# Kernel optimization log

Hardware: AMD Instinct MI355X
Metric: run time of the kernel (lower is better)

Reference implementation:

```python
import jax, jax.numpy as jnp
import numpy as np

B, S, IN_DIM = 2, 2048, 1024
DIMS, QH, KVH = 1024, 16, 4
HD = DIMS // QH          # head_dims = 64
G = QH // KVH            # groups = 4


def setup_inputs() -> dict:
    key = jax.random.key(0)
    k1, k2, k3, k4, k5, k6 = jax.random.split(key, 6)
    scale = 0.02
    q_in = jax.random.normal(k1, (B, S, IN_DIM), dtype=jnp.float32)
    kv_in = jax.random.normal(k2, (B, S, IN_DIM), dtype=jnp.float32)
    # causal mask (True = attend)
    mask = jnp.tril(jnp.ones((S, S), dtype=bool))
    Wq = jax.random.normal(k3, (IN_DIM, QH, HD), dtype=jnp.float32) * scale
    Wk = jax.random.normal(k4, (IN_DIM, KVH, HD), dtype=jnp.float32) * scale
    Wv = jax.random.normal(k5, (IN_DIM, KVH, HD), dtype=jnp.float32) * scale
    Wo = jax.random.normal(k6, (KVH * HD, IN_DIM), dtype=jnp.float32) * scale
    return {"q_in": q_in, "kv_in": kv_in, "mask": mask,
            "Wq": Wq, "Wk": Wk, "Wv": Wv, "Wo": Wo}


def reference(q_in, kv_in, mask, Wq, Wk, Wv, Wo):
    b, s, _ = q_in.shape
    # projections (DenseGeneral, no bias)
    q = jnp.einsum('bsi,ihd->bshd', q_in, Wq)   # [B,S,QH,HD]
    k = jnp.einsum('bsi,ihd->bshd', kv_in, Wk)  # [B,S,KVH,HD]
    v = jnp.einsum('bsi,ihd->bshd', kv_in, Wv)  # [B,S,KVH,HD]
    # rearrange '... s (h g) d -> ... g h s d' with g=G (h outer, g inner),
    # then einsum '... g h s d, ... h a d -> ... h s a' sums over g.
    # Equivalent (and cheaper): sum q over the group axis first.
    q_g = q.reshape(b, s, KVH, G, HD).sum(axis=3)        # [B,S,KVH,HD]
    q_g = jnp.transpose(q_g, (0, 2, 1, 3))               # [B,KVH,S,HD]
    k = jnp.transpose(k, (0, 2, 1, 3))                   # [B,KVH,S,HD]
    v = jnp.transpose(v, (0, 2, 1, 3))                   # [B,KVH,S,HD]
    scores = jnp.einsum('bhsd,bhad->bhsa', q_g, k)       # [B,KVH,S,S]
    scores = jnp.where(mask[None, None, :, :], scores, -jnp.inf)
    attn = jax.nn.softmax(scores / (HD ** 0.5), axis=-1)
    out = jnp.einsum('bhsa,bhad->bhsd', attn, v)         # [B,KVH,S,HD]
    out = jnp.transpose(out, (0, 2, 1, 3)).reshape(b, s, KVH * HD)
    return out @ Wo                                      # [B,S,IN_DIM]
```

## Files before the change

kernel.cpp:

```cpp
#include <hip/hip_runtime.h>
#include <hip/hip_bf16.h>

#define SS 2048
#define NSPLIT 8

typedef __attribute__((ext_vector_type(8))) short bf16x8;
typedef __attribute__((ext_vector_type(4))) float f32x4;

__device__ __forceinline__ short f2bf(float f){
    unsigned u = __float_as_uint(f);
    u += 0x7fff + ((u >> 16) & 1);
    return (short)(u >> 16);
}
__device__ __forceinline__ float bf2f(short s){
    return __uint_as_float(((unsigned)(unsigned short)s) << 16);
}
__device__ __forceinline__ void gload_lds16(const void* g, void* l){
    __builtin_amdgcn_global_load_lds((const __attribute__((address_space(1))) void*)g,
                                     (__attribute__((address_space(3))) void*)l, 16, 0, 0);
}

__global__ __launch_bounds__(256) void k_prep_w(const float* __restrict__ Wq,
                                                const float* __restrict__ Wk,
                                                const float* __restrict__ Wv,
                                                const float* __restrict__ Wo,
                                                const float* __restrict__ q_in,
                                                const float* __restrict__ kv_in,
                                                short* __restrict__ WcatT,
                                                short* __restrict__ WoT,
                                                short* __restrict__ Xb){
    const int bx = blockIdx.x;
    if (bx >= 256) {
        const int b2 = bx - 256;
        const float* src = (b2 < 128) ? q_in : kv_in;
        short* dst = Xb + ((b2 < 128) ? (size_t)0 : (size_t)4194304);
        const int tg = (b2 & 127) * 256 + threadIdx.x;
        #pragma unroll
        for (int j = 0; j < 8; ++j) {
            size_t off = (size_t)tg * 16 + (size_t)j * 524288;
            float4 f0 = *(const float4*)(src + off);
            float4 f1 = *(const float4*)(src + off + 4);
            float4 f2 = *(const float4*)(src + off + 8);
            float4 f3 = *(const float4*)(src + off + 12);
            short t[16];
            t[0]=f2bf(f0.x); t[1]=f2bf(f0.y); t[2]=f2bf(f0.z); t[3]=f2bf(f0.w);
            t[4]=f2bf(f1.x); t[5]=f2bf(f1.y); t[6]=f2bf(f1.z); t[7]=f2bf(f1.w);
            t[8]=f2bf(f2.x); t[9]=f2bf(f2.y); t[10]=f2bf(f2.z); t[11]=f2bf(f2.w);
            t[12]=f2bf(f3.x); t[13]=f2bf(f3.y); t[14]=f2bf(f3.z); t[15]=f2bf(f3.w);
            *(bf16x8*)(dst + off)     = *(bf16x8*)&t[0];
            *(bf16x8*)(dst + off + 8) = *(bf16x8*)&t[8];
        }
        return;
    }
    __shared__ float Ts[64][65];
    const int r  = threadIdx.x >> 2;
    const int cq = (threadIdx.x & 3) * 16;
    if (bx < 192) {
        const int ktile = bx & 15, ntile = bx >> 4;
        const int k0 = ktile * 64, n0 = ntile * 64;
        if (ntile < 4) {
            const float* base = Wq + (size_t)(k0 + r) * 1024 + ntile * 256;
            #pragma unroll
            for (int i = 0; i < 16; i += 4) {
                float4 a = *(const float4*)(base + cq + i);
                float4 b = *(const float4*)(base + 64 + cq + i);
                float4 c = *(const float4*)(base + 128 + cq + i);
                float4 d = *(const float4*)(base + 192 + cq + i);
                Ts[r][cq+i]   = 0.125f * (a.x + b.x + c.x + d.x);
                Ts[r][cq+i+1] = 0.125f * (a.y + b.y + c.y + d.y);
                Ts[r][cq+i+2] = 0.125f * (a.z + b.z + c.z + d.z);
                Ts[r][cq+i+3] = 0.125f * (a.w + b.w + c.w + d.w);
            }
        } else {
            const float* W = (ntile < 8) ? Wk : Wv;
            const float* base = W + (size_t)(k0 + r) * 256 + (ntile & 3) * 64;
            #pragma unroll
            for (int i = 0; i < 16; i += 4) {
                float4 a = *(const float4*)(base + cq + i);
                Ts[r][cq+i] = a.x; Ts[r][cq+i+1] = a.y;
                Ts[r][cq+i+2] = a.z; Ts[r][cq+i+3] = a.w;
            }
        }
        __syncthreads();
        short tmp[16];
        #pragma unroll
        for (int i = 0; i < 16; ++i) tmp[i] = f2bf(Ts[cq+i][r]);
        short* dst = WcatT + (size_t)(n0 + r) * 1024 + k0 + cq;
        *(bf16x8*)dst       = *(bf16x8*)&tmp[0];
        *(bf16x8*)(dst + 8) = *(bf16x8*)&tmp[8];
    } else {
        const int b2 = bx - 192;
        const int ktile = b2 & 3, ntile = b2 >> 2;
        const int k0 = ktile * 64, n0 = ntile * 64;
        const float* base = Wo + (size_t)(k0 + r) * 1024 + n0;
        #pragma unroll
        for (int i = 0; i < 16; i += 4) {
            float4 a = *(const float4*)(base + cq + i);
            Ts[r][cq+i] = a.x; Ts[r][cq+i+1] = a.y;
            Ts[r][cq+i+2] = a.z; Ts[r][cq+i+3] = a.w;
        }
        __syncthreads();
        short tmp[16];
        #pragma unroll
        for (int i = 0; i < 16; ++i) tmp[i] = f2bf(Ts[cq+i][r]);
        short* dst = WoT + (size_t)(n0 + r) * 256 + k0 + cq;
        *(bf16x8*)dst       = *(bf16x8*)&tmp[0];
        *(bf16x8*)(dst + 8) = *(bf16x8*)&tmp[8];
    }
}

__global__ __launch_bounds__(256) void k_gemm1(const short* __restrict__ Xb,
                                               const short* __restrict__ WcatT,
                                               short* __restrict__ pqk,
                                               short* __restrict__ vt){
    const int m0 = blockIdx.x * 128;
    const int n0 = blockIdx.y * 128;
    const short* X = Xb + ((n0 < 256) ? (size_t)0 : (size_t)4194304);
    const int tid = threadIdx.x;
    const int wave = tid >> 6, lane = tid & 63, quad = lane >> 4, l16 = lane & 15;
    const int wrow = (wave & 1) * 64, wcol = (wave >> 1) * 64;

    __shared__ char SMEM[65536];

    f32x4 acc[4][4];
    #pragma unroll
    for (int tm = 0; tm < 4; ++tm)
        #pragma unroll
        for (int tn = 0; tn < 4; ++tn) acc[tm][tn] = f32x4{0.f,0.f,0.f,0.f};

    const int lr8 = lane >> 3;
    const int sb  = ((lane & 7) * 16) ^ (lr8 << 4);
    const char* Abase = (const char*)X     + (size_t)m0 * 2048;
    const char* Bbase = (const char*)WcatT + (size_t)n0 * 2048;

    auto STAGE = [&](int buf, int k0) {
        #pragma unroll
        for (int j = 0; j < 4; ++j) {
            const int row = wave * 32 + j * 8 + lr8;
            const size_t goff = (size_t)row * 2048 + (size_t)k0 * 2 + sb;
            gload_lds16(Abase + goff, SMEM + buf * 32768 + wave * 4096 + j * 1024);
            gload_lds16(Bbase + goff, SMEM + buf * 32768 + 16384 + wave * 4096 + j * 1024);
        }
    };

    STAGE(0, 0);
    for (int k0 = 0; k0 < 1024; k0 += 64) {
        __syncthreads();
        const int cur = (k0 >> 6) & 1;
        if (k0 + 64 < 1024) STAGE(cur ^ 1, k0 + 64);
        #pragma unroll
        for (int ks = 0; ks < 2; ++ks) {
            const int cswz = ((ks * 64 + quad * 16) ^ ((l16 & 7) << 4));
            bf16x8 a[4];
            #pragma unroll
            for (int tm = 0; tm < 4; ++tm) {
                const int R = wrow + tm * 16 + l16;
                a[tm] = *(const bf16x8*)(SMEM + cur * 32768 + R * 128 + cswz);
            }
            #pragma unroll
            for (int tn = 0; tn < 4; ++tn) {
                const int R2 = wcol + tn * 16 + l16;
                bf16x8 b = *(const bf16x8*)(SMEM + cur * 32768 + 16384 + R2 * 128 + cswz);
                #pragma unroll
                for (int tm = 0; tm < 4; ++tm)
                    acc[tm][tn] = __builtin_amdgcn_mfma_f32_16x16x32_bf16(a[tm], b, acc[tm][tn], 0, 0, 0);
            }
        }
    }
    __syncthreads();

    if (n0 < 512) {
        #pragma unroll
        for (int tm = 0; tm < 4; ++tm) {
            const int mrow = m0 + wrow + tm * 16 + quad * 4;
            #pragma unroll
            for (int tn = 0; tn < 4; ++tn) {
                const int col = n0 + wcol + tn * 16 + l16;
                #pragma unroll
                for (int rg = 0; rg < 4; ++rg)
                    pqk[(size_t)(mrow + rg) * 512 + col] = f2bf(acc[tm][tn][rg]);
            }
        }
    } else {
        short* SM16 = (short*)SMEM;
        #pragma unroll
        for (int tm = 0; tm < 4; ++tm) {
            const int ml = wrow + tm * 16 + quad * 4;
            #pragma unroll
            for (int tn = 0; tn < 4; ++tn) {
                const int cl = wcol + tn * 16 + l16;
                #pragma unroll
                for (int rg = 0; rg < 4; ++rg)
                    SM16[cl * 136 + ml + rg] = f2bf(acc[tm][tn][rg]);
            }
        }
        __syncthreads();
        const int row  = tid >> 1;
        const int half = tid & 1;
        const int colv = (n0 - 512) + row;
        const int vh = colv >> 6, d = colv & 63;
        const int batch = m0 >> 11;
        const int s0 = (m0 & 2047) + half * 64;
        short* dst = vt + ((size_t)((batch * 4 + vh) * 64 + d)) * 2048 + s0;
        const short* src = &SM16[row * 136 + half * 64];
        #pragma unroll
        for (int i = 0; i < 64; i += 8)
            *(bf16x8*)(dst + i) = *(const bf16x8*)(src + i);
    }
}

__global__ __launch_bounds__(256) void k_attn4(const short* __restrict__ pqk,
                                               const short* __restrict__ vt,
                                               short* __restrict__ Op,
                                               float* __restrict__ Lp){
    const int bx = blockIdx.x;
    const int qt = 31 - (bx / NSPLIT);
    const int s  = bx - (bx / NSPLIT) * NSPLIT;
    const int kv = blockIdx.y, batch = blockIdx.z;
    const int tid = threadIdx.x;
    const int wave = tid >> 6, lane = tid & 63, quad = lane >> 4, l16 = lane & 15;
    const int r = tid >> 2, c = (tid & 3) * 16;
    const int part = (((batch * 4 + kv) * 32 + qt) * NSPLIT + s);

    __shared__ short Ks[64][72];
    __shared__ short Vs[64][72];
    __shared__ short Ps[64][72];

    const size_t qrow = (size_t)(batch * SS + qt * 64 + wave * 16 + l16);
    bf16x8 aq0 = *(const bf16x8*)(pqk + qrow * 512 + kv * 64 + quad * 8);
    bf16x8 aq1 = *(const bf16x8*)(pqk + qrow * 512 + kv * 64 + 32 + quad * 8);

    f32x4 accO[4];
    #pragma unroll
    for (int t = 0; t < 4; ++t) accO[t] = f32x4{0.f, 0.f, 0.f, 0.f};
    float lrow[4] = {0.f, 0.f, 0.f, 0.f};

    bf16x8 rk0, rk1, rv0, rv1;
    int kt = s;
    if (kt <= qt) {
        const short* ksrc = pqk + (size_t)(batch * SS + kt * 64 + r) * 512 + 256 + kv * 64 + c;
        rk0 = *(const bf16x8*)ksrc; rk1 = *(const bf16x8*)(ksrc + 8);
        const short* vsrc = vt + ((size_t)((batch * 4 + kv) * 64 + r)) * 2048 + kt * 64 + c;
        rv0 = *(const bf16x8*)vsrc; rv1 = *(const bf16x8*)(vsrc + 8);
    }
    for (; kt <= qt; kt += NSPLIT) {
        *(bf16x8*)&Ks[r][c]     = rk0;
        *(bf16x8*)&Ks[r][c + 8] = rk1;
        *(bf16x8*)&Vs[r][c]     = rv0;
        *(bf16x8*)&Vs[r][c + 8] = rv1;
        __syncthreads();
        if (kt + NSPLIT <= qt) {
            const short* ksrc = pqk + (size_t)(batch * SS + (kt + NSPLIT) * 64 + r) * 512 + 256 + kv * 64 + c;
            rk0 = *(const bf16x8*)ksrc; rk1 = *(const bf16x8*)(ksrc + 8);
            const short* vsrc = vt + ((size_t)((batch * 4 + kv) * 64 + r)) * 2048 + (kt + NSPLIT) * 64 + c;
            rv0 = *(const bf16x8*)vsrc; rv1 = *(const bf16x8*)(vsrc + 8);
        }

        f32x4 sc[4];
        #pragma unroll
        for (int t = 0; t < 4; ++t) sc[t] = f32x4{0.f, 0.f, 0.f, 0.f};
        #pragma unroll
        for (int ks = 0; ks < 2; ++ks) {
            bf16x8 a = ks ? aq1 : aq0;
            #pragma unroll
            for (int t = 0; t < 4; ++t) {
                bf16x8 b = *(bf16x8*)&Ks[t * 16 + l16][ks * 32 + quad * 8];
                sc[t] = __builtin_amdgcn_mfma_f32_16x16x32_bf16(a, b, sc[t], 0, 0, 0);
            }
        }
        if (kt == qt) {
            #pragma unroll
            for (int t = 0; t < 4; ++t) {
                int colg = t * 16 + l16;
                #pragma unroll
                for (int rg = 0; rg < 4; ++rg)
                    if (colg > wave * 16 + quad * 4 + rg) sc[t][rg] = -1e30f;
            }
        }
        #pragma unroll
        for (int t = 0; t < 4; ++t) {
            #pragma unroll
            for (int rg = 0; rg < 4; ++rg) {
                float p = __expf(sc[t][rg]);
                lrow[rg] += p;
                Ps[wave * 16 + quad * 4 + rg][t * 16 + l16] = f2bf(p);
            }
        }
        #pragma unroll
        for (int ks = 0; ks < 2; ++ks) {
            bf16x8 ap = *(bf16x8*)&Ps[wave * 16 + l16][ks * 32 + quad * 8];
            #pragma unroll
            for (int t = 0; t < 4; ++t) {
                bf16x8 bv = *(bf16x8*)&Vs[t * 16 + l16][ks * 32 + quad * 8];
                accO[t] = __builtin_amdgcn_mfma_f32_16x16x32_bf16(ap, bv, accO[t], 0, 0, 0);
            }
        }
        __syncthreads();
    }
    #pragma unroll
    for (int rg = 0; rg < 4; ++rg) {
        float l = lrow[rg];
        l += __shfl_xor(l, 1);
        l += __shfl_xor(l, 2);
        l += __shfl_xor(l, 4);
        l += __shfl_xor(l, 8);
        lrow[rg] = l;
    }
    #pragma unroll
    for (int rg = 0; rg < 4; ++rg) {
        int row = wave * 16 + quad * 4 + rg;
        #pragma unroll
        for (int t = 0; t < 4; ++t)
            Op[(size_t)part * 4096 + row * 64 + t * 16 + l16] = f2bf(accO[t][rg]);
    }
    if (l16 == 0) {
        #pragma unroll
        for (int rg = 0; rg < 4; ++rg)
            Lp[part * 64 + (wave * 16 + quad * 4 + rg)] = lrow[rg];
    }
}

__global__ __launch_bounds__(256) void k_combine(const short* __restrict__ Op,
                                                 const float* __restrict__ Lp,
                                                 short* __restrict__ ao){
    const int qt = blockIdx.x, kv = blockIdx.y, batch = blockIdx.z;
    const int tid = threadIdx.x;
    const int rr = tid >> 2, cs = (tid & 3) * 16;
    const int pbase = ((batch * 4 + kv) * 32 + qt) * NSPLIT;
    float lsum = 0.f;
    #pragma unroll
    for (int i = 0; i < NSPLIT; ++i) lsum += Lp[(pbase + i) * 64 + rr];
    float inv = 1.f / lsum;
    float o[16];
    #pragma unroll
    for (int j = 0; j < 16; ++j) o[j] = 0.f;
    #pragma unroll
    for (int i = 0; i < NSPLIT; ++i) {
        const short* src = Op + (size_t)(pbase + i) * 4096 + rr * 64 + cs;
        bf16x8 v0 = *(const bf16x8*)src;
        bf16x8 v1 = *(const bf16x8*)(src + 8);
        #pragma unroll
        for (int j = 0; j < 8; ++j) { o[j] += bf2f(v0[j]); o[j + 8] += bf2f(v1[j]); }
    }
    short* dst = ao + (size_t)(batch * SS + qt * 64 + rr) * 256 + kv * 64 + cs;
    #pragma unroll
    for (int j = 0; j < 16; ++j)
        dst[j] = f2bf(o[j] * inv);
}

__global__ __launch_bounds__(256) void k_gemm2(const short* __restrict__ ao,
                                               const short* __restrict__ WoT,
                                               float* __restrict__ out){
    const int m0 = blockIdx.x * 128;
    const int n0 = blockIdx.y * 128;
    const int tid = threadIdx.x;
    const int wave = tid >> 6, lane = tid & 63, quad = lane >> 4, l16 = lane & 15;
    const int wrow = (wave & 1) * 64, wcol = (wave >> 1) * 64;
    const int r = tid >> 2, cc = (tid & 3) * 16;

    __shared__ short As[128][72];
    __shared__ short Bs[128][72];

    f32x4 acc[4][4];
    #pragma unroll
    for (int tm = 0; tm < 4; ++tm)
        #pragma unroll
        for (int tn = 0; tn < 4; ++tn) acc[tm][tn] = f32x4{0.f,0.f,0.f,0.f};

    bf16x8 ra0, ra1, ra2, ra3, rb0, rb1, rb2, rb3;
    {
        const short* a0 = ao + (size_t)(m0 + r) * 256 + cc;
        const short* a1 = a0 + (size_t)64 * 256;
        const short* b0 = WoT + (size_t)(n0 + r) * 256 + cc;
        const short* b1 = b0 + (size_t)64 * 256;
        ra0 = *(const bf16x8*)a0; ra1 = *(const bf16x8*)(a0 + 8);
        ra2 = *(const bf16x8*)a1; ra3 = *(const bf16x8*)(a1 + 8);
        rb0 = *(const bf16x8*)b0; rb1 = *(const bf16x8*)(b0 + 8);
        rb2 = *(const bf16x8*)b1; rb3 = *(const bf16x8*)(b1 + 8);
    }
    for (int k0 = 0; k0 < 256; k0 += 64) {
        *(bf16x8*)&As[r][cc]          = ra0;
        *(bf16x8*)&As[r][cc + 8]      = ra1;
        *(bf16x8*)&As[r + 64][cc]     = ra2;
        *(bf16x8*)&As[r + 64][cc + 8] = ra3;
        *(bf16x8*)&Bs[r][cc]          = rb0;
        *(bf16x8*)&Bs[r][cc + 8]      = rb1;
        *(bf16x8*)&Bs[r + 64][cc]     = rb2;
        *(bf16x8*)&Bs[r + 64][cc + 8] = rb3;
        __syncthreads();
        if (k0 + 64 < 256) {
            const short* a0 = ao + (size_t)(m0 + r) * 256 + k0 + 64 + cc;
            const short* a1 = a0 + (size_t)64 * 256;
            const short* b0 = WoT + (size_t)(n0 + r) * 256 + k0 + 64 + cc;
            const short* b1 = b0 + (size_t)64 * 256;
            ra0 = *(const bf16x8*)a0; ra1 = *(const bf16x8*)(a0 + 8);
            ra2 = *(const bf16x8*)a1; ra3 = *(const bf16x8*)(a1 + 8);
            rb0 = *(const bf16x8*)b0; rb1 = *(const bf16x8*)(b0 + 8);
            rb2 = *(const bf16x8*)b1; rb3 = *(const bf16x8*)(b1 + 8);
        }
        #pragma unroll
        for (int ks = 0; ks < 2; ++ks) {
            bf16x8 a[4];
            #pragma unroll
            for (int tm = 0; tm < 4; ++tm)
                a[tm] = *(bf16x8*)&As[wrow + tm * 16 + l16][ks * 32 + quad * 8];
            #pragma unroll
            for (int tn = 0; tn < 4; ++tn) {
                bf16x8 b = *(bf16x8*)&Bs[wcol + tn * 16 + l16][ks * 32 + quad * 8];
                #pragma unroll
                for (int tm = 0; tm < 4; ++tm)
                    acc[tm][tn] = __builtin_amdgcn_mfma_f32_16x16x32_bf16(a[tm], b, acc[tm][tn], 0, 0, 0);
            }
        }
        __syncthreads();
    }
    #pragma unroll
    for (int tm = 0; tm < 4; ++tm) {
        const int mrow = m0 + wrow + tm * 16 + quad * 4;
        #pragma unroll
        for (int tn = 0; tn < 4; ++tn) {
            const int col = n0 + wcol + tn * 16 + l16;
            #pragma unroll
            for (int rg = 0; rg < 4; ++rg)
                out[(size_t)(mrow + rg) * 1024 + col] = acc[tm][tn][rg];
        }
    }
}

extern "C" void kernel_launch(void* const* d_in, const int* in_sizes, int n_in,
                              void* d_out, int out_size, void* d_ws, size_t ws_size,
                              hipStream_t stream) {
    const float* q_in  = (const float*)d_in[0];
    const float* kv_in = (const float*)d_in[1];
    int wqi = 3;
    for (int i = 2; i < n_in; ++i)
        if (in_sizes[i] == 1024 * 16 * 64) { wqi = i; break; }
    const float* Wq = (const float*)d_in[wqi];
    const float* Wk = (const float*)d_in[wqi + 1];
    const float* Wv = (const float*)d_in[wqi + 2];
    const float* Wo = (const float*)d_in[wqi + 3];
    float* out = (float*)d_out;

    char* ws = (char*)d_ws;
    short* WcatT = (short*)(ws);
    short* WoT   = (short*)(ws + 1572864);
    short* ao    = (short*)(ws + 2097152);
    short* pqk   = (short*)(ws + 4194304);
    short* vt    = (short*)(ws + 8388608);
    float* Lp    = (float*)(ws + 10485760);
    short* Op    = (short*)(ws + 33554432);
    short* Xb    = (short*)(ws + 50331648);

    hipLaunchKernelGGL(k_prep_w,  dim3(512),     dim3(256), 0, stream,
                       Wq, Wk, Wv, Wo, q_in, kv_in, WcatT, WoT, Xb);
    hipLaunchKernelGGL(k_gemm1,   dim3(32, 6),   dim3(256), 0, stream,
                       Xb, WcatT, pqk, vt);
    hipLaunchKernelGGL(k_attn4,   dim3(32 * NSPLIT, 4, 2), dim3(256), 0, stream,
                       pqk, vt, Op, Lp);
    hipLaunchKernelGGL(k_combine, dim3(32, 4, 2), dim3(256), 0, stream,
                       Op, Lp, ao);
    hipLaunchKernelGGL(k_gemm2,   dim3(32, 8),   dim3(256), 0, stream,
                       ao, WoT, out);
}
```

Before: 146.6 us.

## Remove split-KV attention and combine kernel, normalize output inside attention

Drops the split-K/V scheme: each block now handles one query tile, loops over all causal key tiles and writes normalized output straight into the attention buffer. This removes the separate combine kernel along with the write and re-read of the partial output and row-sum buffers. In exchange the grid shrinks from 2048 to 256 blocks, and under the causal mask the last query tiles run up to 32 serial iterations, so load balance and latency hiding may get worse.

```diff
diff --git a/kernel.cpp b/kernel.cpp
--- a/kernel.cpp
+++ b/kernel.cpp
@@ -2,7 +2,6 @@
 #include <hip/hip_bf16.h>
 
 #define SS 2048
-#define NSPLIT 8
 
 typedef __attribute__((ext_vector_type(8))) short bf16x8;
 typedef __attribute__((ext_vector_type(4))) float f32x4;
@@ -209,18 +208,14 @@
     }
 }
 
-__global__ __launch_bounds__(256) void k_attn4(const short* __restrict__ pqk,
-                                               const short* __restrict__ vt,
-                                               short* __restrict__ Op,
-                                               float* __restrict__ Lp){
-    const int bx = blockIdx.x;
-    const int qt = 31 - (bx / NSPLIT);
-    const int s  = bx - (bx / NSPLIT) * NSPLIT;
+__global__ __launch_bounds__(256) void k_attn(const short* __restrict__ pqk,
+                                              const short* __restrict__ vt,
+                                              short* __restrict__ ao){
+    const int qt = blockIdx.x;
     const int kv = blockIdx.y, batch = blockIdx.z;
     const int tid = threadIdx.x;
     const int wave = tid >> 6, lane = tid & 63, quad = lane >> 4, l16 = lane & 15;
     const int r = tid >> 2, c = (tid & 3) * 16;
-    const int part = (((batch * 4 + kv) * 32 + qt) * NSPLIT + s);
 
     __shared__ short Ks[64][72];
     __shared__ short Vs[64][72];
@@ -236,23 +231,22 @@
     float lrow[4] = {0.f, 0.f, 0.f, 0.f};
 
     bf16x8 rk0, rk1, rv0, rv1;
-    int kt = s;
-    if (kt <= qt) {
-        const short* ksrc = pqk + (size_t)(batch * SS + kt * 64 + r) * 512 + 256 + kv * 64 + c;
+    {
+        const short* ksrc = pqk + (size_t)(batch * SS + r) * 512 + 256 + kv * 64 + c;
         rk0 = *(const bf16x8*)ksrc; rk1 = *(const bf16x8*)(ksrc + 8);
-        const short* vsrc = vt + ((size_t)((batch * 4 + kv) * 64 + r)) * 2048 + kt * 64 + c;
+        const short* vsrc = vt + ((size_t)((batch * 4 + kv) * 64 + r)) * 2048 + c;
         rv0 = *(const bf16x8*)vsrc; rv1 = *(const bf16x8*)(vsrc + 8);
     }
-    for (; kt <= qt; kt += NSPLIT) {
+    for (int kt = 0; kt <= qt; ++kt) {
         *(bf16x8*)&Ks[r][c]     = rk0;
         *(bf16x8*)&Ks[r][c + 8] = rk1;
         *(bf16x8*)&Vs[r][c]     = rv0;
         *(bf16x8*)&Vs[r][c + 8] = rv1;
         __syncthreads();
-        if (kt + NSPLIT <= qt) {
-            const short* ksrc = pqk + (size_t)(batch * SS + (kt + NSPLIT) * 64 + r) * 512 + 256 + kv * 64 + c;
+        if (kt + 1 <= qt) {
+            const short* ksrc = pqk + (size_t)(batch * SS + (kt + 1) * 64 + r) * 512 + 256 + kv * 64 + c;
             rk0 = *(const bf16x8*)ksrc; rk1 = *(const bf16x8*)(ksrc + 8);
-            const short* vsrc = vt + ((size_t)((batch * 4 + kv) * 64 + r)) * 2048 + (kt + NSPLIT) * 64 + c;
+            const short* vsrc = vt + ((size_t)((batch * 4 + kv) * 64 + r)) * 2048 + (kt + 1) * 64 + c;
             rv0 = *(const bf16x8*)vsrc; rv1 = *(const bf16x8*)(vsrc + 8);
         }
 
@@ -304,48 +298,16 @@
         l += __shfl_xor(l, 2);
         l += __shfl_xor(l, 4);
         l += __shfl_xor(l, 8);
-        lrow[rg] = l;
+        lrow[rg] = 1.f / l;
     }
     #pragma unroll
     for (int rg = 0; rg < 4; ++rg) {
-        int row = wave * 16 + quad * 4 + rg;
+        const int row = qt * 64 + wave * 16 + quad * 4 + rg;
+        short* dst = ao + (size_t)(batch * SS + row) * 256 + kv * 64;
         #pragma unroll
         for (int t = 0; t < 4; ++t)
-            Op[(size_t)part * 4096 + row * 64 + t * 16 + l16] = f2bf(accO[t][rg]);
-    }
-    if (l16 == 0) {
-        #pragma unroll
-        for (int rg = 0; rg < 4; ++rg)
-            Lp[part * 64 + (wave * 16 + quad * 4 + rg)] = lrow[rg];
-    }
-}
-
-__global__ __launch_bounds__(256) void k_combine(const short* __restrict__ Op,
-                                                 const float* __restrict__ Lp,
-                                                 short* __restrict__ ao){
-    const int qt = blockIdx.x, kv = blockIdx.y, batch = blockIdx.z;
-    const int tid = threadIdx.x;
-    const int rr = tid >> 2, cs = (tid & 3) * 16;
-    const int pbase = ((batch * 4 + kv) * 32 + qt) * NSPLIT;
-    float lsum = 0.f;
-    #pragma unroll
-    for (int i = 0; i < NSPLIT; ++i) lsum += Lp[(pbase + i) * 64 + rr];
-    float inv = 1.f / lsum;
-    float o[16];
-    #pragma unroll
-    for (int j = 0; j < 16; ++j) o[j] = 0.f;
-    #pragma unroll
-    for (int i = 0; i < NSPLIT; ++i) {
-        const short* src = Op + (size_t)(pbase + i) * 4096 + rr * 64 + cs;
-        bf16x8 v0 = *(const bf16x8*)src;
-        bf16x8 v1 = *(const bf16x8*)(src + 8);
-        #pragma unroll
-        for (int j = 0; j < 8; ++j) { o[j] += bf2f(v0[j]); o[j + 8] += bf2f(v1[j]); }
-    }
-    short* dst = ao + (size_t)(batch * SS + qt * 64 + rr) * 256 + kv * 64 + cs;
-    #pragma unroll
-    for (int j = 0; j < 16; ++j)
-        dst[j] = f2bf(o[j] * inv);
+            dst[t * 16 + l16] = f2bf(accO[t][rg] * lrow[rg]);
+    }
 }
 
 __global__ __launch_bounds__(256) void k_gemm2(const short* __restrict__ ao,
@@ -447,18 +409,14 @@
     short* ao    = (short*)(ws + 2097152);
     short* pqk   = (short*)(ws + 4194304);
     short* vt    = (short*)(ws + 8388608);
-    float* Lp    = (float*)(ws + 10485760);
-    short* Op    = (short*)(ws + 33554432);
     short* Xb    = (short*)(ws + 50331648);
 
     hipLaunchKernelGGL(k_prep_w,  dim3(512),     dim3(256), 0, stream,
                        Wq, Wk, Wv, Wo, q_in, kv_in, WcatT, WoT, Xb);
     hipLaunchKernelGGL(k_gemm1,   dim3(32, 6),   dim3(256), 0, stream,
                        Xb, WcatT, pqk, vt);
-    hipLaunchKernelGGL(k_attn4,   dim3(32 * NSPLIT, 4, 2), dim3(256), 0, stream,
-                       pqk, vt, Op, Lp);
-    hipLaunchKernelGGL(k_combine, dim3(32, 4, 2), dim3(256), 0, stream,
-                       Op, Lp, ao);
+    hipLaunchKernelGGL(k_attn,    dim3(32, 4, 2), dim3(256), 0, stream,
+                       pqk, vt, ao);
     hipLaunchKernelGGL(k_gemm2,   dim3(32, 8),   dim3(256), 0, stream,
                        ao, WoT, out);
 }
```

After: 154.0 us. 5.0% more time.

## Fuse split-KV combine into attention via last-block atomic counter

Applied to the files above, without the earlier changes.

Removes the separate combine kernel launch: each attention block increments a per-query-tile atomic counter after writing its partial output, and the last finishing split reduces all partials and writes the normalized result. Counters are zeroed in the prep kernel. This saves a kernel launch and its dependency gap, at the cost of a threadfence plus atomic per block and a serial tail in the last block of each group.

```diff
diff --git a/kernel.cpp b/kernel.cpp
--- a/kernel.cpp
+++ b/kernel.cpp
@@ -28,9 +28,11 @@
                                                 const float* __restrict__ kv_in,
                                                 short* __restrict__ WcatT,
                                                 short* __restrict__ WoT,
-                                                short* __restrict__ Xb){
+                                                short* __restrict__ Xb,
+                                                unsigned* __restrict__ cnt){
     const int bx = blockIdx.x;
     if (bx >= 256) {
+        if (bx == 256 && threadIdx.x < 256) cnt[threadIdx.x] = 0u;
         const int b2 = bx - 256;
         const float* src = (b2 < 128) ? q_in : kv_in;
         short* dst = Xb + ((b2 < 128) ? (size_t)0 : (size_t)4194304);
@@ -212,7 +214,9 @@
 __global__ __launch_bounds__(256) void k_attn4(const short* __restrict__ pqk,
                                                const short* __restrict__ vt,
                                                short* __restrict__ Op,
-                                               float* __restrict__ Lp){
+                                               float* __restrict__ Lp,
+                                               unsigned* __restrict__ cnt,
+                                               short* __restrict__ ao){
     const int bx = blockIdx.x;
     const int qt = 31 - (bx / NSPLIT);
     const int s  = bx - (bx / NSPLIT) * NSPLIT;
@@ -220,11 +224,13 @@
     const int tid = threadIdx.x;
     const int wave = tid >> 6, lane = tid & 63, quad = lane >> 4, l16 = lane & 15;
     const int r = tid >> 2, c = (tid & 3) * 16;
-    const int part = (((batch * 4 + kv) * 32 + qt) * NSPLIT + s);
+    const int grp  = ((batch * 4 + kv) * 32 + qt);
+    const int part = grp * NSPLIT + s;
 
     __shared__ short Ks[64][72];
     __shared__ short Vs[64][72];
     __shared__ short Ps[64][72];
+    __shared__ int s_old;
 
     const size_t qrow = (size_t)(batch * SS + qt * 64 + wave * 16 + l16);
     bf16x8 aq0 = *(const bf16x8*)(pqk + qrow * 512 + kv * 64 + quad * 8);
@@ -318,34 +324,35 @@
         for (int rg = 0; rg < 4; ++rg)
             Lp[part * 64 + (wave * 16 + quad * 4 + rg)] = lrow[rg];
     }
-}
-
-__global__ __launch_bounds__(256) void k_combine(const short* __restrict__ Op,
-                                                 const float* __restrict__ Lp,
-                                                 short* __restrict__ ao){
-    const int qt = blockIdx.x, kv = blockIdx.y, batch = blockIdx.z;
-    const int tid = threadIdx.x;
-    const int rr = tid >> 2, cs = (tid & 3) * 16;
-    const int pbase = ((batch * 4 + kv) * 32 + qt) * NSPLIT;
-    float lsum = 0.f;
-    #pragma unroll
-    for (int i = 0; i < NSPLIT; ++i) lsum += Lp[(pbase + i) * 64 + rr];
-    float inv = 1.f / lsum;
-    float o[16];
-    #pragma unroll
-    for (int j = 0; j < 16; ++j) o[j] = 0.f;
-    #pragma unroll
-    for (int i = 0; i < NSPLIT; ++i) {
-        const short* src = Op + (size_t)(pbase + i) * 4096 + rr * 64 + cs;
-        bf16x8 v0 = *(const bf16x8*)src;
-        bf16x8 v1 = *(const bf16x8*)(src + 8);
-        #pragma unroll
-        for (int j = 0; j < 8; ++j) { o[j] += bf2f(v0[j]); o[j + 8] += bf2f(v1[j]); }
-    }
-    short* dst = ao + (size_t)(batch * SS + qt * 64 + rr) * 256 + kv * 64 + cs;
-    #pragma unroll
-    for (int j = 0; j < 16; ++j)
-        dst[j] = f2bf(o[j] * inv);
+
+    __threadfence();
+    __syncthreads();
+    if (tid == 0) s_old = (int)atomicAdd(&cnt[grp], 1u);
+    __syncthreads();
+    if (s_old == NSPLIT - 1) {
+        __threadfence();
+        const int rr = tid >> 2, cs = (tid & 3) * 16;
+        const int pbase = grp * NSPLIT;
+        float lsum = 0.f;
+        #pragma unroll
+        for (int i = 0; i < NSPLIT; ++i) lsum += Lp[(pbase + i) * 64 + rr];
+        float inv = 1.f / lsum;
+        float o[16];
+        #pragma unroll
+        for (int j = 0; j < 16; ++j) o[j] = 0.f;
+        #pragma unroll
+        for (int i = 0; i < NSPLIT; ++i) {
+            const short* src = Op + (size_t)(pbase + i) * 4096 + rr * 64 + cs;
+            bf16x8 v0 = *(const bf16x8*)src;
+            bf16x8 v1 = *(const bf16x8*)(src + 8);
+            #pragma unroll
+            for (int j = 0; j < 8; ++j) { o[j] += bf2f(v0[j]); o[j + 8] += bf2f(v1[j]); }
+        }
+        short* dst = ao + (size_t)(batch * SS + qt * 64 + rr) * 256 + kv * 64 + cs;
+        #pragma unroll
+        for (int j = 0; j < 16; ++j)
+            dst[j] = f2bf(o[j] * inv);
+    }
 }
 
 __global__ __launch_bounds__(256) void k_gemm2(const short* __restrict__ ao,
@@ -442,23 +449,22 @@
     float* out = (float*)d_out;
 
     char* ws = (char*)d_ws;
-    short* WcatT = (short*)(ws);
-    short* WoT   = (short*)(ws + 1572864);
-    short* ao    = (short*)(ws + 2097152);
-    short* pqk   = (short*)(ws + 4194304);
-    short* vt    = (short*)(ws + 8388608);
-    float* Lp    = (float*)(ws + 10485760);
-    short* Op    = (short*)(ws + 33554432);
-    short* Xb    = (short*)(ws + 50331648);
+    short* WcatT    = (short*)(ws);
+    short* WoT      = (short*)(ws + 1572864);
+    short* ao       = (short*)(ws + 2097152);
+    short* pqk      = (short*)(ws + 4194304);
+    short* vt       = (short*)(ws + 8388608);
+    float* Lp       = (float*)(ws + 10485760);
+    unsigned* cnt   = (unsigned*)(ws + 11534336);
+    short* Op       = (short*)(ws + 33554432);
+    short* Xb       = (short*)(ws + 50331648);
 
     hipLaunchKernelGGL(k_prep_w,  dim3(512),     dim3(256), 0, stream,
-                       Wq, Wk, Wv, Wo, q_in, kv_in, WcatT, WoT, Xb);
+                       Wq, Wk, Wv, Wo, q_in, kv_in, WcatT, WoT, Xb, cnt);
     hipLaunchKernelGGL(k_gemm1,   dim3(32, 6),   dim3(256), 0, stream,
                        Xb, WcatT, pqk, vt);
     hipLaunchKernelGGL(k_attn4,   dim3(32 * NSPLIT, 4, 2), dim3(256), 0, stream,
-                       pqk, vt, Op, Lp);
-    hipLaunchKernelGGL(k_combine, dim3(32, 4, 2), dim3(256), 0, stream,
-                       Op, Lp, ao);
+                       pqk, vt, Op, Lp, cnt, ao);
     hipLaunchKernelGGL(k_gemm2,   dim3(32, 8),   dim3(256), 0, stream,
                        ao, WoT, out);
 }
```

After: 479.3 us. 227% more time.

## Load K/V MFMA fragments directly from global memory, dropping LDS staging and barriers

Applied to the files above, without the earlier changes.

The attention kernel no longer stages K and V tiles in shared memory. Each wave now reads its K and V MFMA operand fragments straight from global memory, which removes both per-iteration __syncthreads. The P tile stays in LDS but is only touched by its own wave. In exchange, every wave fetches the same K/V data separately (roughly four times the cache traffic), the reads are strided rather than coalesced, and the register prefetch of the next tile is gone, so load latency sits inside the loop.

```diff
diff --git a/kernel.cpp b/kernel.cpp
--- a/kernel.cpp
+++ b/kernel.cpp
@@ -219,43 +219,24 @@
     const int kv = blockIdx.y, batch = blockIdx.z;
     const int tid = threadIdx.x;
     const int wave = tid >> 6, lane = tid & 63, quad = lane >> 4, l16 = lane & 15;
-    const int r = tid >> 2, c = (tid & 3) * 16;
     const int part = (((batch * 4 + kv) * 32 + qt) * NSPLIT + s);
 
-    __shared__ short Ks[64][72];
-    __shared__ short Vs[64][72];
     __shared__ short Ps[64][72];
 
     const size_t qrow = (size_t)(batch * SS + qt * 64 + wave * 16 + l16);
     bf16x8 aq0 = *(const bf16x8*)(pqk + qrow * 512 + kv * 64 + quad * 8);
     bf16x8 aq1 = *(const bf16x8*)(pqk + qrow * 512 + kv * 64 + 32 + quad * 8);
 
+    const short* Kb = pqk + (size_t)(batch * SS) * 512 + 256 + kv * 64
+                    + (size_t)(l16) * 512 + quad * 8;
+    const short* Vb = vt + ((size_t)((batch * 4 + kv) * 64 + l16)) * 2048 + quad * 8;
+
     f32x4 accO[4];
     #pragma unroll
     for (int t = 0; t < 4; ++t) accO[t] = f32x4{0.f, 0.f, 0.f, 0.f};
     float lrow[4] = {0.f, 0.f, 0.f, 0.f};
 
-    bf16x8 rk0, rk1, rv0, rv1;
-    int kt = s;
-    if (kt <= qt) {
-        const short* ksrc = pqk + (size_t)(batch * SS + kt * 64 + r) * 512 + 256 + kv * 64 + c;
-        rk0 = *(const bf16x8*)ksrc; rk1 = *(const bf16x8*)(ksrc + 8);
-        const short* vsrc = vt + ((size_t)((batch * 4 + kv) * 64 + r)) * 2048 + kt * 64 + c;
-        rv0 = *(const bf16x8*)vsrc; rv1 = *(const bf16x8*)(vsrc + 8);
-    }
-    for (; kt <= qt; kt += NSPLIT) {
-        *(bf16x8*)&Ks[r][c]     = rk0;
-        *(bf16x8*)&Ks[r][c + 8] = rk1;
-        *(bf16x8*)&Vs[r][c]     = rv0;
-        *(bf16x8*)&Vs[r][c + 8] = rv1;
-        __syncthreads();
-        if (kt + NSPLIT <= qt) {
-            const short* ksrc = pqk + (size_t)(batch * SS + (kt + NSPLIT) * 64 + r) * 512 + 256 + kv * 64 + c;
-            rk0 = *(const bf16x8*)ksrc; rk1 = *(const bf16x8*)(ksrc + 8);
-            const short* vsrc = vt + ((size_t)((batch * 4 + kv) * 64 + r)) * 2048 + (kt + NSPLIT) * 64 + c;
-            rv0 = *(const bf16x8*)vsrc; rv1 = *(const bf16x8*)(vsrc + 8);
-        }
-
+    for (int kt = s; kt <= qt; kt += NSPLIT) {
         f32x4 sc[4];
         #pragma unroll
         for (int t = 0; t < 4; ++t) sc[t] = f32x4{0.f, 0.f, 0.f, 0.f};
@@ -264,10 +245,16 @@
             bf16x8 a = ks ? aq1 : aq0;
             #pragma unroll
             for (int t = 0; t < 4; ++t) {
-                bf16x8 b = *(bf16x8*)&Ks[t * 16 + l16][ks * 32 + quad * 8];
+                bf16x8 b = *(const bf16x8*)(Kb + (size_t)(kt * 64 + t * 16) * 512 + ks * 32);
                 sc[t] = __builtin_amdgcn_mfma_f32_16x16x32_bf16(a, b, sc[t], 0, 0, 0);
             }
         }
+        bf16x8 bv[2][4];
+        #pragma unroll
+        for (int ks = 0; ks < 2; ++ks)
+            #pragma unroll
+            for (int t = 0; t < 4; ++t)
+                bv[ks][t] = *(const bf16x8*)(Vb + (size_t)(t * 16) * 2048 + kt * 64 + ks * 32);
         if (kt == qt) {
             #pragma unroll
             for (int t = 0; t < 4; ++t) {
@@ -290,12 +277,9 @@
         for (int ks = 0; ks < 2; ++ks) {
             bf16x8 ap = *(bf16x8*)&Ps[wave * 16 + l16][ks * 32 + quad * 8];
             #pragma unroll
-            for (int t = 0; t < 4; ++t) {
-                bf16x8 bv = *(bf16x8*)&Vs[t * 16 + l16][ks * 32 + quad * 8];
-                accO[t] = __builtin_amdgcn_mfma_f32_16x16x32_bf16(ap, bv, accO[t], 0, 0, 0);
-            }
-        }
-        __syncthreads();
+            for (int t = 0; t < 4; ++t)
+                accO[t] = __builtin_amdgcn_mfma_f32_16x16x32_bf16(ap, bv[ks][t], accO[t], 0, 0, 0);
+        }
     }
     #pragma unroll
     for (int rg = 0; rg < 4; ++rg) {
```

After: 175.0 us. 1.19x slower.
